# Performance work log

Hardware: AMD Instinct MI355X
Metric: run time of the kernel (lower is better)

Reference implementation:

```python
import jax, jax.numpy as jnp
import numpy as np

STACK = 4

def setup_inputs() -> dict:
    key = jax.random.key(0)
    k1, k2, k3 = jax.random.split(key, 3)
    b, t, c = 16, 3000, 80
    proj_dim, num_codes = 16, 8192
    x = jax.random.normal(k1, (b, t, c), dtype=jnp.float32)
    # xavier_uniform for proj: bound = sqrt(6/(fan_in+fan_out))
    fan_in, fan_out = c * STACK, proj_dim
    bound = float(np.sqrt(6.0 / (fan_in + fan_out)))
    proj = jax.random.uniform(k2, (fan_in, proj_dim), dtype=jnp.float32,
                              minval=-bound, maxval=bound)
    codebook = jax.random.normal(k3, (num_codes, proj_dim), dtype=jnp.float32)
    return {"x": x, "proj": proj, "codebook": codebook}

def _l2norm(v, axis=-1, eps=1e-12):
    # matches torch F.normalize(dim=-1)
    n = jnp.sqrt(jnp.sum(v * v, axis=axis, keepdims=True))
    return v / jnp.maximum(n, eps)

def reference(x, proj, codebook):
    b, t, c = x.shape
    if STACK > 1:
        pad = (STACK - t % STACK) % STACK
        if pad:
            x = jnp.pad(x, ((0, 0), (0, pad), (0, 0)))
            t = x.shape[1]
        x = x.reshape(b, t // STACK, c * STACK)
    x_proj = _l2norm(x @ proj)                 # (b, t', proj_dim)
    cb = _l2norm(codebook)                     # (num_codes, proj_dim)
    # ||a-c||^2 = ||a||^2 + ||c||^2 - 2 a.c = 2 - 2 a.c for unit vectors;
    # avoids materializing the (b, t', num_codes, proj_dim) diff tensor.
    scores = jnp.einsum('btd,nd->btn', x_proj, cb)  # (b, t', num_codes)
    dist = 2.0 - 2.0 * scores
    return jnp.argmin(dist, axis=-1)
```

## Files before the change

### kernel.cpp

```cpp
#include <hip/hip_runtime.h>


#define ROWS   12000
#define DIN    320
#define PD     16
#define NCODES 8192

#define NSL    8
#define SLC    (NCODES/NSL)
#define RT     6
#define RPB    48
#define NRG    (ROWS/RPB)
#define GRID   (NRG*NSL)

typedef unsigned long long u64;

__global__ __launch_bounds__(256) void prep_pt(const float* __restrict__ proj,
                                               float* __restrict__ projT) {
    int gt = blockIdx.x * 256 + threadIdx.x;
    if (gt < DIN * PD) {
        int k = gt >> 4, p = gt & 15;
        projT[p * DIN + k] = proj[k * PD + p];
    }
}

__global__ __launch_bounds__(256) void prep_cb(const float* __restrict__ cb,
                                               float* __restrict__ cbt) {
    int gt = blockIdx.x * 256 + threadIdx.x;
    int n = gt >> 4, p = gt & 15;
    float v = cb[gt];
    float ss = v * v;
    ss += __shfl_xor(ss, 1, 16);
    ss += __shfl_xor(ss, 2, 16);
    ss += __shfl_xor(ss, 4, 16);
    ss += __shfl_xor(ss, 8, 16);
    float nrm = fmaxf(sqrtf(ss), 1e-12f);
    int s = n >> 10, cl = n & 1023, q = p >> 2, j = p & 3;
    cbt[s * 16384 + q * 4096 + cl * 4 + j] = v / nrm;
}

__global__ __launch_bounds__(256) void prep_xp(const float* __restrict__ x,
                                               const float* __restrict__ projT,
                                               float* __restrict__ xp) {
    int gt = blockIdx.x * 256 + threadIdx.x;
    int r = gt >> 4, p = gt & 15;
    const float4* xr = reinterpret_cast<const float4*>(x + (size_t)r * DIN);
    const float4* pt = reinterpret_cast<const float4*>(projT + (size_t)p * DIN);
    float acc = 0.f;
#pragma unroll 8
    for (int k4 = 0; k4 < DIN / 4; ++k4) {
        float4 xv = xr[k4];
        float4 pv = pt[k4];
        acc = fmaf(xv.x, pv.x, acc);
        acc = fmaf(xv.y, pv.y, acc);
        acc = fmaf(xv.z, pv.z, acc);
        acc = fmaf(xv.w, pv.w, acc);
    }
    float ss = acc * acc;
    ss += __shfl_xor(ss, 1, 16);
    ss += __shfl_xor(ss, 2, 16);
    ss += __shfl_xor(ss, 4, 16);
    ss += __shfl_xor(ss, 8, 16);
    xp[gt] = acc / fmaxf(sqrtf(ss), 1e-12f);
}

__global__ __launch_bounds__(256)
__attribute__((amdgpu_waves_per_eu(2, 2)))
void rpq_main(const float* __restrict__ xp,
              const float* __restrict__ cbt,
              u64* __restrict__ keys) {
    __shared__ __align__(16) float4 lds4[SLC * PD / 4];

    const int tid   = threadIdx.x;
    const int cs    = tid & 31;
    const int rs    = tid >> 5;
    const int slice = blockIdx.x & (NSL - 1);
    const int rg    = blockIdx.x >> 3;
    const int row0  = rg * RPB + rs * RT;

    {
        const float4* src = reinterpret_cast<const float4*>(cbt) + (size_t)slice * (SLC * PD / 4);
#pragma unroll
        for (int it = 0; it < 16; ++it)
            lds4[it * 256 + tid] = src[it * 256 + tid];
    }

    float4 xq[RT][4];
#pragma unroll
    for (int r = 0; r < RT; ++r) {
        const float4* s4 = reinterpret_cast<const float4*>(xp + (size_t)(row0 + r) * PD);
#pragma unroll
        for (int q = 0; q < 4; ++q) xq[r][q] = s4[q];
    }

    float bd[RT];
    int   bi[RT];
#pragma unroll
    for (int r = 0; r < RT; ++r) { bd[r] = 3.0e38f; bi[r] = 0; }

    __syncthreads();

    const float4* base = lds4 + cs;
    const int code_base = slice * SLC;

#pragma unroll 4
    for (int i = 0; i < SLC / 32; ++i) {
        const float4 c0 = base[i * 32 +    0];
        const float4 c1 = base[i * 32 + 1024];
        const float4 c2 = base[i * 32 + 2048];
        const float4 c3 = base[i * 32 + 3072];
        const int gcode = code_base + i * 32 + cs;
#pragma unroll
        for (int r = 0; r < RT; ++r) {
            float s = 0.f;
            s = fmaf(xq[r][0].x, c0.x, s); s = fmaf(xq[r][0].y, c0.y, s);
            s = fmaf(xq[r][0].z, c0.z, s); s = fmaf(xq[r][0].w, c0.w, s);
            s = fmaf(xq[r][1].x, c1.x, s); s = fmaf(xq[r][1].y, c1.y, s);
            s = fmaf(xq[r][1].z, c1.z, s); s = fmaf(xq[r][1].w, c1.w, s);
            s = fmaf(xq[r][2].x, c2.x, s); s = fmaf(xq[r][2].y, c2.y, s);
            s = fmaf(xq[r][2].z, c2.z, s); s = fmaf(xq[r][2].w, c2.w, s);
            s = fmaf(xq[r][3].x, c3.x, s); s = fmaf(xq[r][3].y, c3.y, s);
            s = fmaf(xq[r][3].z, c3.z, s); s = fmaf(xq[r][3].w, c3.w, s);
            float dd = 2.0f - 2.0f * s;
            if (dd < bd[r]) { bd[r] = dd; bi[r] = gcode; }
        }
    }

#pragma unroll
    for (int r = 0; r < RT; ++r) {
        unsigned ub = __float_as_uint(bd[r]);
        ub = (ub & 0x80000000u) ? ~ub : (ub | 0x80000000u);
        u64 key = ((u64)ub << 32) | (unsigned)bi[r];
#pragma unroll
        for (int off = 16; off >= 1; off >>= 1) {
            u64 o = __shfl_xor(key, off, 32);
            key = (o < key) ? o : key;
        }
        if (cs == 0) keys[(size_t)slice * ROWS + row0 + r] = key;
    }
}

__global__ __launch_bounds__(256) void rpq_reduce(const u64* __restrict__ keys,
                                                  int* __restrict__ out) {
    int r = blockIdx.x * 256 + threadIdx.x;
    if (r >= ROWS) return;
    u64 m = keys[r];
#pragma unroll
    for (int s = 1; s < NSL; ++s) {
        u64 o = keys[(size_t)s * ROWS + r];
        m = (o < m) ? o : m;
    }
    out[r] = (int)(m & 0xFFFFFFFFu);
}

extern "C" void kernel_launch(void* const* d_in, const int* in_sizes, int n_in,
                              void* d_out, int out_size, void* d_ws, size_t ws_size,
                              hipStream_t stream) {
    const float* x    = (const float*)d_in[0];
    const float* proj = (const float*)d_in[1];
    const float* cb   = (const float*)d_in[2];
    int* out = (int*)d_out;

    float* cbt   = (float*)d_ws;
    float* xp    = (float*)((char*)d_ws + 524288);
    float* projT = (float*)((char*)d_ws + 524288 + 786432);
    u64*   keys  = (u64*)  ((char*)d_ws + 524288 + 786432 + 32768);

    prep_pt<<<(DIN * PD + 255) / 256, 256, 0, stream>>>(proj, projT);
    prep_cb<<<(NCODES * PD) / 256, 256, 0, stream>>>(cb, cbt);
    prep_xp<<<(ROWS * PD) / 256, 256, 0, stream>>>(x, projT, xp);
    rpq_main<<<GRID, 256, 0, stream>>>(xp, cbt, keys);
    rpq_reduce<<<(ROWS + 255) / 256, 256, 0, stream>>>(keys, out);
}
```

Baseline: 147.1 us.

## Split codebook into 16 slices, raise occupancy, fuse projection transpose into per-row prep

```diff
diff --git a/kernel.cpp b/kernel.cpp
--- a/kernel.cpp
+++ b/kernel.cpp
@@ -6,7 +6,7 @@
 #define PD     16
 #define NCODES 8192
 
-#define NSL    8
+#define NSL    16
 #define SLC    (NCODES/NSL)
 #define RT     6
 #define RPB    48
@@ -14,15 +14,6 @@
 #define GRID   (NRG*NSL)
 
 typedef unsigned long long u64;
-
-__global__ __launch_bounds__(256) void prep_pt(const float* __restrict__ proj,
-                                               float* __restrict__ projT) {
-    int gt = blockIdx.x * 256 + threadIdx.x;
-    if (gt < DIN * PD) {
-        int k = gt >> 4, p = gt & 15;
-        projT[p * DIN + k] = proj[k * PD + p];
-    }
-}
 
 __global__ __launch_bounds__(256) void prep_cb(const float* __restrict__ cb,
                                                float* __restrict__ cbt) {
@@ -35,37 +26,68 @@
     ss += __shfl_xor(ss, 4, 16);
     ss += __shfl_xor(ss, 8, 16);
     float nrm = fmaxf(sqrtf(ss), 1e-12f);
-    int s = n >> 10, cl = n & 1023, q = p >> 2, j = p & 3;
-    cbt[s * 16384 + q * 4096 + cl * 4 + j] = v / nrm;
+    int s = n >> 9, cl = n & 511, q = p >> 2, j = p & 3;
+    cbt[s * 8192 + q * 2048 + cl * 4 + j] = v / nrm;
 }
 
-__global__ __launch_bounds__(256) void prep_xp(const float* __restrict__ x,
-                                               const float* __restrict__ projT,
-                                               float* __restrict__ xp) {
-    int gt = blockIdx.x * 256 + threadIdx.x;
-    int r = gt >> 4, p = gt & 15;
+__global__ __launch_bounds__(64) void prep_xp(const float* __restrict__ x,
+                                              const float* __restrict__ proj,
+                                              float* __restrict__ xp) {
+    int r = blockIdx.x * 64 + threadIdx.x;
+    if (r >= ROWS) return;
     const float4* xr = reinterpret_cast<const float4*>(x + (size_t)r * DIN);
-    const float4* pt = reinterpret_cast<const float4*>(projT + (size_t)p * DIN);
-    float acc = 0.f;
-#pragma unroll 8
+    const float4* pr = reinterpret_cast<const float4*>(proj);
+
+    float acc[PD];
+#pragma unroll
+    for (int p = 0; p < PD; ++p) acc[p] = 0.f;
+
+#pragma unroll 4
     for (int k4 = 0; k4 < DIN / 4; ++k4) {
         float4 xv = xr[k4];
-        float4 pv = pt[k4];
-        acc = fmaf(xv.x, pv.x, acc);
-        acc = fmaf(xv.y, pv.y, acc);
-        acc = fmaf(xv.z, pv.z, acc);
-        acc = fmaf(xv.w, pv.w, acc);
+#pragma unroll
+        for (int j = 0; j < 4; ++j) {
+            float xs = (j == 0) ? xv.x : (j == 1) ? xv.y : (j == 2) ? xv.z : xv.w;
+            const float4* prow = pr + (size_t)(k4 * 4 + j) * 4;
+            float4 p0 = prow[0], p1 = prow[1], p2 = prow[2], p3 = prow[3];
+            acc[ 0] = fmaf(xs, p0.x, acc[ 0]); acc[ 1] = fmaf(xs, p0.y, acc[ 1]);
+            acc[ 2] = fmaf(xs, p0.z, acc[ 2]); acc[ 3] = fmaf(xs, p0.w, acc[ 3]);
+            acc[ 4] = fmaf(xs, p1.x, acc[ 4]); acc[ 5] = fmaf(xs, p1.y, acc[ 5]);
+            acc[ 6] = fmaf(xs, p1.z, acc[ 6]); acc[ 7] = fmaf(xs, p1.w, acc[ 7]);
+            acc[ 8] = fmaf(xs, p2.x, acc[ 8]); acc[ 9] = fmaf(xs, p2.y, acc[ 9]);
+            acc[10] = fmaf(xs, p2.z, acc[10]); acc[11] = fmaf(xs, p2.w, acc[11]);
+            acc[12] = fmaf(xs, p3.x, acc[12]); acc[13] = fmaf(xs, p3.y, acc[13]);
+            acc[14] = fmaf(xs, p3.z, acc[14]); acc[15] = fmaf(xs, p3.w, acc[15]);
+        }
     }
-    float ss = acc * acc;
-    ss += __shfl_xor(ss, 1, 16);
-    ss += __shfl_xor(ss, 2, 16);
-    ss += __shfl_xor(ss, 4, 16);
-    ss += __shfl_xor(ss, 8, 16);
-    xp[gt] = acc / fmaxf(sqrtf(ss), 1e-12f);
+
+    float sq[PD];
+#pragma unroll
+    for (int p = 0; p < PD; ++p) sq[p] = acc[p] * acc[p];
+    float t1[8], t2[4], t3[2];
+#pragma unroll
+    for (int i = 0; i < 8; ++i) t1[i] = sq[2 * i] + sq[2 * i + 1];
+#pragma unroll
+    for (int i = 0; i < 4; ++i) t2[i] = t1[2 * i] + t1[2 * i + 1];
+#pragma unroll
+    for (int i = 0; i < 2; ++i) t3[i] = t2[2 * i] + t2[2 * i + 1];
+    float ss = t3[0] + t3[1];
+    float nrm = fmaxf(sqrtf(ss), 1e-12f);
+
+    float4* dst = reinterpret_cast<float4*>(xp + (size_t)r * PD);
+#pragma unroll
+    for (int q = 0; q < 4; ++q) {
+        float4 o;
+        o.x = acc[q * 4 + 0] / nrm;
+        o.y = acc[q * 4 + 1] / nrm;
+        o.z = acc[q * 4 + 2] / nrm;
+        o.w = acc[q * 4 + 3] / nrm;
+        dst[q] = o;
+    }
 }
 
 __global__ __launch_bounds__(256)
-__attribute__((amdgpu_waves_per_eu(2, 2)))
+__attribute__((amdgpu_waves_per_eu(4, 4)))
 void rpq_main(const float* __restrict__ xp,
               const float* __restrict__ cbt,
               u64* __restrict__ keys) {
@@ -75,13 +97,13 @@
     const int cs    = tid & 31;
     const int rs    = tid >> 5;
     const int slice = blockIdx.x & (NSL - 1);
-    const int rg    = blockIdx.x >> 3;
+    const int rg    = blockIdx.x >> 4;
     const int row0  = rg * RPB + rs * RT;
 
     {
         const float4* src = reinterpret_cast<const float4*>(cbt) + (size_t)slice * (SLC * PD / 4);
 #pragma unroll
-        for (int it = 0; it < 16; ++it)
+        for (int it = 0; it < 8; ++it)
             lds4[it * 256 + tid] = src[it * 256 + tid];
     }
 
@@ -106,9 +128,9 @@
 #pragma unroll 4
     for (int i = 0; i < SLC / 32; ++i) {
         const float4 c0 = base[i * 32 +    0];
-        const float4 c1 = base[i * 32 + 1024];
-        const float4 c2 = base[i * 32 + 2048];
-        const float4 c3 = base[i * 32 + 3072];
+        const float4 c1 = base[i * 32 +  512];
+        const float4 c2 = base[i * 32 + 1024];
+        const float4 c3 = base[i * 32 + 1536];
         const int gcode = code_base + i * 32 + cs;
 #pragma unroll
         for (int r = 0; r < RT; ++r) {
@@ -161,14 +183,12 @@
     const float* cb   = (const float*)d_in[2];
     int* out = (int*)d_out;
 
-    float* cbt   = (float*)d_ws;
-    float* xp    = (float*)((char*)d_ws + 524288);
-    float* projT = (float*)((char*)d_ws + 524288 + 786432);
-    u64*   keys  = (u64*)  ((char*)d_ws + 524288 + 786432 + 32768);
+    float* cbt  = (float*)d_ws;
+    float* xp   = (float*)((char*)d_ws + 524288);
+    u64*   keys = (u64*)  ((char*)d_ws + 524288 + 786432);
 
-    prep_pt<<<(DIN * PD + 255) / 256, 256, 0, stream>>>(proj, projT);
     prep_cb<<<(NCODES * PD) / 256, 256, 0, stream>>>(cb, cbt);
-    prep_xp<<<(ROWS * PD) / 256, 256, 0, stream>>>(x, projT, xp);
+    prep_xp<<<(ROWS + 63) / 64, 64, 0, stream>>>(x, proj, xp);
     rpq_main<<<GRID, 256, 0, stream>>>(xp, cbt, keys);
     rpq_reduce<<<(ROWS + 255) / 256, 256, 0, stream>>>(keys, out);
 }
```

New measurement: 470.3 us. 220% more time.
